# Performance work log

Hardware: AMD Instinct MI355X
Metric: run time of the kernel (lower is better)

The kernel has to match this reference:

```python
import jax, jax.numpy as jnp
import numpy as np

B, S, D = 32, 512, 1024
H, DH = 16, 64
EPS, TEMP = 1e-7, 0.1
P_LOGIT_INIT = float(np.log(0.2) - np.log(0.8))  # init_min == init_max == 0.2


def setup_inputs() -> dict:
    key = jax.random.key(0)
    ks = jax.random.split(key, 10)
    x = jax.random.normal(ks[0], (B, S, D), dtype=jnp.float32)
    lengths_x = jax.random.randint(ks[1], (B,), 0, S - 1)
    lengths_x = lengths_x.at[0].set(S - 1)  # ensure max(lengths)+1 == S, as torch code assumes
    Wq = jax.random.normal(ks[2], (D, H * DH), dtype=jnp.float32) * 0.02
    Wk = jax.random.normal(ks[3], (D, H * DH), dtype=jnp.float32) * 0.02
    Wv = jax.random.normal(ks[4], (D, H * DH), dtype=jnp.float32) * 0.02
    Wo = jax.random.normal(ks[5], (H * DH, D), dtype=jnp.float32) * 0.02
    p_logits = jnp.full((4,), P_LOGIT_INIT, dtype=jnp.float32)  # q, k, v, o
    noise_q = jax.random.uniform(ks[6], (B, S, D), dtype=jnp.float32)
    noise_k = jax.random.uniform(ks[7], (B, S, D), dtype=jnp.float32)
    noise_v = jax.random.uniform(ks[8], (B, S, D), dtype=jnp.float32)
    noise_o = jax.random.uniform(ks[9], (B, S, H * DH), dtype=jnp.float32)
    return {"x": x, "lengths_x": lengths_x, "Wq": Wq, "Wk": Wk, "Wv": Wv,
            "Wo": Wo, "p_logits": p_logits, "noise_q": noise_q,
            "noise_k": noise_k, "noise_v": noise_v, "noise_o": noise_o}


def _concrete_dropout(x, p_logit, u):
    p = jax.nn.sigmoid(p_logit)
    drop_prob = jax.nn.sigmoid(
        (jnp.log(p + EPS) - jnp.log(1.0 - p + EPS)
         + jnp.log(u + EPS) - jnp.log(1.0 - u + EPS)) / TEMP)
    return x * (1.0 - drop_prob) / (1.0 - p)


def reference(x, lengths_x, Wq, Wk, Wv, Wo, p_logits, noise_q, noise_k, noise_v, noise_o):
    b, s, _ = x.shape
    q = (_concrete_dropout(x, p_logits[0], noise_q) @ Wq).reshape(b, s, H, DH)
    k = (_concrete_dropout(x, p_logits[1], noise_k) @ Wk).reshape(b, s, H, DH)
    v = (_concrete_dropout(x, p_logits[2], noise_v) @ Wv).reshape(b, s, H, DH)
    e = jnp.einsum('bxhd,byhd->bhxy', q, k) / np.sqrt(DH).astype(np.float32)
    # mask[b, i, j] = 1 iff i <= lengths[b] and j <= lengths[b]
    valid = jnp.arange(s)[None, :] <= lengths_x[:, None]          # [B, S]
    mask = (valid[:, :, None] & valid[:, None, :])[:, None, :, :]  # [B, 1, S, S]
    e = jnp.where(mask, e, jnp.float32(-1e10))
    alpha = jax.nn.softmax(e, axis=-1)                             # [B, H, S, S]
    out = jnp.einsum('bhxy,byhd->bxhd', alpha, v).reshape(b, s, H * DH)
    out = _concrete_dropout(out, p_logits[3], noise_o) @ Wo
    return jax.nn.relu(out), alpha
```

## Files before the change

kernel.cpp:

```cpp
#include <hip/hip_runtime.h>

constexpr int B_ = 32, S_ = 512, D_ = 1024, H_ = 16, DH_ = 64, HD_ = 1024;
constexpr int M_ = B_ * S_;
constexpr float EPS_ = 1e-7f;
constexpr float INV_TEMP_ = 10.0f;

typedef __attribute__((ext_vector_type(8))) short bf16x8;
typedef __attribute__((ext_vector_type(4))) short bf16x4;
typedef __attribute__((ext_vector_type(4))) float f32x4;
typedef __attribute__((ext_vector_type(8))) unsigned short us8;

__device__ __forceinline__ float sigm(float x) { return 1.0f / (1.0f + __expf(-x)); }

__device__ __forceinline__ unsigned short f2bf(float f) {
    unsigned u = __float_as_uint(f);
    unsigned r = (u + 0x7FFFu + ((u >> 16) & 1u)) >> 16;
    return (unsigned short)r;
}

#define GLL16(gp, lp) __builtin_amdgcn_global_load_lds( \
    (const __attribute__((address_space(1))) unsigned int*)(gp), \
    (__attribute__((address_space(3))) unsigned int*)(lp), 16, 0, 0)

__device__ __forceinline__ bf16x8 ldsfrag64(const unsigned short* base, int row, int k) {
    int slot = ((k >> 3) ^ (row & 7)) << 3;
    return *(const bf16x8*)(base + row * 64 + slot);
}

__global__ __launch_bounds__(256)
void cd_cast3_kernel(const float* __restrict__ x,
                     const float* __restrict__ nq, const float* __restrict__ nk,
                     const float* __restrict__ nv, const float* __restrict__ pl,
                     unsigned short* __restrict__ aq, unsigned short* __restrict__ ak,
                     unsigned short* __restrict__ av)
{
    size_t i0 = ((size_t)blockIdx.x * 256 + threadIdx.x) * 8;

    float c0[3], inv1mp[3];
#pragma unroll
    for (int j = 0; j < 3; ++j) {
        float p = sigm(pl[j]);
        c0[j] = __logf(p + EPS_) - __logf(1.0f - p + EPS_);
        inv1mp[j] = 1.0f / (1.0f - p);
    }

    float4 x0 = *(const float4*)(x + i0);
    float4 x1 = *(const float4*)(x + i0 + 4);
    float xv[8] = {x0.x, x0.y, x0.z, x0.w, x1.x, x1.y, x1.z, x1.w};

    const float* ns[3] = {nq, nk, nv};
    unsigned short* os[3] = {aq, ak, av};
#pragma unroll
    for (int j = 0; j < 3; ++j) {
        float4 u0 = *(const float4*)(ns[j] + i0);
        float4 u1 = *(const float4*)(ns[j] + i0 + 4);
        float uv[8] = {u0.x, u0.y, u0.z, u0.w, u1.x, u1.y, u1.z, u1.w};
        ushort out[8];
#pragma unroll
        for (int t = 0; t < 8; ++t) {
            float lt = (c0[j] + __logf(uv[t] + EPS_) - __logf(1.0f - uv[t] + EPS_)) * INV_TEMP_;
            float dpr = sigm(lt);
            out[t] = f2bf(xv[t] * (1.0f - dpr) * inv1mp[j]);
        }
        *(us8*)(os[j] + i0) = *(us8*)out;
    }
}

__global__ __launch_bounds__(256)
void wcast_t4_kernel(const float* __restrict__ W0, const float* __restrict__ W1,
                     const float* __restrict__ W2, const float* __restrict__ W3,
                     unsigned short* __restrict__ T0, unsigned short* __restrict__ T1,
                     unsigned short* __restrict__ T2, unsigned short* __restrict__ T3)
{
    __shared__ unsigned short t[64][72];
    int z = blockIdx.z;
    const float* W = (z & 2) ? ((z & 1) ? W3 : W2) : ((z & 1) ? W1 : W0);
    unsigned short* WT = (z & 2) ? ((z & 1) ? T3 : T2) : ((z & 1) ? T1 : T0);
    int kb = blockIdx.y * 64;
    int nb = blockIdx.x * 64;
    int tid = threadIdx.x;
#pragma unroll
    for (int i = 0; i < 4; ++i) {
        int idx = tid + i * 256;
        int r = idx >> 4, c4 = idx & 15;
        float4 v = *(const float4*)(W + (size_t)(kb + r) * 1024 + nb + c4 * 4);
        t[c4 * 4 + 0][r] = f2bf(v.x);
        t[c4 * 4 + 1][r] = f2bf(v.y);
        t[c4 * 4 + 2][r] = f2bf(v.z);
        t[c4 * 4 + 3][r] = f2bf(v.w);
    }
    __syncthreads();
#pragma unroll
    for (int i = 0; i < 4; ++i) {
        int idx = tid + i * 256;
        int r = idx >> 4, c4 = idx & 15;
        ushort4 o;
        o.x = t[r][c4 * 4 + 0];
        o.y = t[r][c4 * 4 + 1];
        o.z = t[r][c4 * 4 + 2];
        o.w = t[r][c4 * 4 + 3];
        *(ushort4*)(WT + (size_t)(nb + r) * 1024 + kb + c4 * 4) = o;
    }
}

__global__ __launch_bounds__(256)
void vtrans_kernel(const unsigned short* __restrict__ vb, unsigned short* __restrict__ vT)
{
    __shared__ unsigned short t[64][136];
    int bh = blockIdx.y, b = bh >> 4, h = bh & 15;
    int y0 = blockIdx.x * 128;
    int tid = threadIdx.x;
#pragma unroll
    for (int i = 0; i < 4; ++i) {
        int idx = tid + i * 256;
        int r = idx >> 3, d0 = (idx & 7) * 8;
        us8 v = *(const us8*)(vb + ((size_t)(b * 512 + y0 + r)) * 1024 + h * 64 + d0);
#pragma unroll
        for (int e = 0; e < 8; ++e) t[d0 + e][r] = v[e];
    }
    __syncthreads();
#pragma unroll
    for (int i = 0; i < 4; ++i) {
        int idx = tid + i * 256;
        int dr = idx >> 4, y4 = (idx & 15) * 8;
        us8 o = *(const us8*)&t[dr][y4];
        *(us8*)(vT + ((size_t)bh * 64 + dr) * 512 + y0 + y4) = o;
    }
}

template<bool RELU, bool BF16OUT>
__global__ __launch_bounds__(256, 3)
void gemm_bf16_kernel(const unsigned short* __restrict__ A,
                      const unsigned short* __restrict__ BT,
                      void* __restrict__ Cv)
{
    const size_t zo = (size_t)blockIdx.y;
    A  += zo * (size_t)M_ * HD_;
    BT += zo * (size_t)(1024 * 1024);

    __shared__ unsigned short As[128 * 32];
    __shared__ unsigned short Bs[128 * 32];

    int flat = blockIdx.x;
    int swz = (flat & 7) * 128 + (flat >> 3);
    int ntile = swz & 7, mtile = swz >> 3;
    int m0 = mtile * 128, n0 = ntile * 128;

    int tid = threadIdx.x;
    int w = tid >> 6, lane = tid & 63;
    int wm = w >> 1, wn = w & 1;

    f32x4 acc[4][4];
#pragma unroll
    for (int m = 0; m < 4; ++m)
#pragma unroll
        for (int n = 0; n < 4; ++n) acc[m][n] = (f32x4){0.f, 0.f, 0.f, 0.f};

    const unsigned short* Ag = A + (size_t)(m0 + w * 32 + (lane >> 2)) * 1024 + (lane & 3) * 8;
    const unsigned short* Bg = BT + (size_t)(n0 + w * 32 + (lane >> 2)) * 1024 + (lane & 3) * 8;
    unsigned short* AsW = As + (w * 32) * 32;
    unsigned short* BsW = Bs + (w * 32) * 32;

    const int arow = wm * 64 + (lane & 15);
    const int brow = wn * 64 + (lane & 15);
    const int koff = (lane >> 4) * 8;

    for (int k0 = 0; k0 < 1024; k0 += 32) {
        __syncthreads();
        GLL16(Ag + k0,             AsW);
        GLL16(Ag + k0 + 16 * 1024, AsW + 16 * 32);
        GLL16(Bg + k0,             BsW);
        GLL16(Bg + k0 + 16 * 1024, BsW + 16 * 32);
        __syncthreads();

        bf16x8 afr[4], bfr[4];
#pragma unroll
        for (int m = 0; m < 4; ++m)
            afr[m] = *(const bf16x8*)&As[(arow + m * 16) * 32 + koff];
#pragma unroll
        for (int n = 0; n < 4; ++n)
            bfr[n] = *(const bf16x8*)&Bs[(brow + n * 16) * 32 + koff];
#pragma unroll
        for (int m = 0; m < 4; ++m)
#pragma unroll
            for (int n = 0; n < 4; ++n)
                acc[m][n] = __builtin_amdgcn_mfma_f32_16x16x32_bf16(afr[m], bfr[n], acc[m][n], 0, 0, 0);
    }

    int cr = (lane >> 4) * 4, cc = lane & 15;
#pragma unroll
    for (int m = 0; m < 4; ++m)
#pragma unroll
        for (int n = 0; n < 4; ++n)
#pragma unroll
            for (int j = 0; j < 4; ++j) {
                int row = m0 + wm * 64 + m * 16 + cr + j;
                int col = n0 + wn * 64 + n * 16 + cc;
                float v = acc[m][n][j];
                if (RELU) v = fmaxf(v, 0.f);
                if (BF16OUT) ((unsigned short*)Cv)[zo * (size_t)M_ * HD_ + (size_t)row * 1024 + col] = f2bf(v);
                else         ((float*)Cv)[(size_t)row * 1024 + col] = v;
            }
}

__global__ __launch_bounds__(512, 2)
void fused_attn2_kernel(const unsigned short* __restrict__ qb,
                        const unsigned short* __restrict__ kb,
                        const unsigned short* __restrict__ vT,
                        const float* __restrict__ no,
                        const float* __restrict__ pl,
                        const int* __restrict__ lengths,
                        float* __restrict__ alpha,
                        unsigned short* __restrict__ Ao)
{
    const int bh = blockIdx.x;
    const int b = bh >> 4, h = bh & 15;
    const int tid = threadIdx.x;
    const int w = tid >> 6, lane = tid & 63;
    const int g = lane >> 4, li = lane & 15;
    const int len = lengths[b];

    __shared__ unsigned short Kall[512 * 64];
    __shared__ unsigned short Vall[8 * 64 * 64];
    __shared__ unsigned short Olb[128 * 72];

    const int sr = lane >> 3;
    const int sc = ((lane & 7) ^ sr) * 8;

    {
        const size_t kbase = ((size_t)(b * 512 + w * 64)) * 1024 + h * 64;
        const size_t vbase = ((size_t)bh * 64) * 512;
#pragma unroll
        for (int c = 0; c < 8; ++c) {
            GLL16(kb + kbase + (size_t)(c * 8 + sr) * 1024 + sc, Kall + w * 4096 + c * 512);
            GLL16(vT + vbase + (size_t)(c * 8 + sr) * 512 + w * 64 + sc, Vall + w * 4096 + c * 512);
        }
    }
    __syncthreads();

    const float po = sigm(pl[3]);
    const float c0o = __logf(po + EPS_) - __logf(1.0f - po + EPS_);
    const float inv1mpo = 1.0f / (1.0f - po);

    for (int qt = 0; qt < 4; ++qt) {
        const int xg = qt * 128 + w * 16 + li;

        const unsigned short* qp = qb + ((size_t)(b * 512 + xg)) * 1024 + h * 64 + g * 8;
        bf16x8 qf0 = *(const bf16x8*)qp;
        bf16x8 qf1 = *(const bf16x8*)(qp + 32);

        f32x4 acc[32];
#pragma unroll
        for (int f = 0; f < 32; ++f) acc[f] = (f32x4){0.f, 0.f, 0.f, 0.f};

#pragma unroll
        for (int f = 0; f < 32; ++f) {
            bf16x8 kf0 = ldsfrag64(Kall, f * 16 + li, g * 8);
            bf16x8 kf1 = ldsfrag64(Kall, f * 16 + li, g * 8 + 32);
            acc[f] = __builtin_amdgcn_mfma_f32_16x16x32_bf16(kf0, qf0, acc[f], 0, 0, 0);
            acc[f] = __builtin_amdgcn_mfma_f32_16x16x32_bf16(kf1, qf1, acc[f], 0, 0, 0);
        }

        const bool vx = (xg <= len);
        float mx = -3.4e38f;
#pragma unroll
        for (int f = 0; f < 32; ++f)
#pragma unroll
            for (int r = 0; r < 4; ++r) {
                int y = f * 16 + g * 4 + r;
                float s = (vx && (y <= len)) ? acc[f][r] * 0.125f : -1e10f;
                acc[f][r] = s;
                mx = fmaxf(mx, s);
            }
        mx = fmaxf(mx, __shfl_xor(mx, 16));
        mx = fmaxf(mx, __shfl_xor(mx, 32));
        float sum = 0.f;
#pragma unroll
        for (int f = 0; f < 32; ++f)
#pragma unroll
            for (int r = 0; r < 4; ++r) {
                float e = __expf(acc[f][r] - mx);
                acc[f][r] = e;
                sum += e;
            }
        sum += __shfl_xor(sum, 16);
        sum += __shfl_xor(sum, 32);
        const float inv = 1.0f / sum;

        float* arow = alpha + ((size_t)bh * 512 + xg) * 512;
#pragma unroll
        for (int f = 0; f < 32; ++f) {
            f32x4 av = acc[f];
            av[0] *= inv; av[1] *= inv; av[2] *= inv; av[3] *= inv;
            acc[f] = av;
            *(float4*)(arow + f * 16 + g * 4) = make_float4(av[0], av[1], av[2], av[3]);
        }

        f32x4 acco[4];
#pragma unroll
        for (int cf = 0; cf < 4; ++cf) acco[cf] = (f32x4){0.f, 0.f, 0.f, 0.f};

#pragma unroll
        for (int yt = 0; yt < 8; ++yt) {
            const unsigned short* Vc = Vall + yt * 4096;
#pragma unroll
            for (int w2 = 0; w2 < 2; ++w2) {
                int f0 = yt * 4 + w2 * 2;
                bf16x8 pf;
#pragma unroll
                for (int r = 0; r < 4; ++r) {
                    pf[r]     = (short)f2bf(acc[f0][r]);
                    pf[4 + r] = (short)f2bf(acc[f0 + 1][r]);
                }
#pragma unroll
                for (int cf = 0; cf < 4; ++cf) {
                    int d = cf * 16 + li;
                    int s0 = w2 * 8 + g;
                    int s1 = s0 + 4;
                    int p0 = (((s0 >> 1) ^ (d & 7)) << 3) + ((s0 & 1) << 2);
                    int p1 = (((s1 >> 1) ^ (d & 7)) << 3) + ((s1 & 1) << 2);
                    bf16x4 lo = *(const bf16x4*)(Vc + d * 64 + p0);
                    bf16x4 hi = *(const bf16x4*)(Vc + d * 64 + p1);
                    bf16x8 vf;
#pragma unroll
                    for (int e = 0; e < 4; ++e) { vf[e] = lo[e]; vf[4 + e] = hi[e]; }
                    acco[cf] = __builtin_amdgcn_mfma_f32_16x16x32_bf16(pf, vf, acco[cf], 0, 0, 0);
                }
            }
        }

#pragma unroll
        for (int cf = 0; cf < 4; ++cf)
#pragma unroll
            for (int r = 0; r < 4; ++r)
                Olb[(w * 16 + g * 4 + r) * 72 + cf * 16 + li] = f2bf(acco[cf][r]);
        __syncthreads();

#pragma unroll
        for (int i = 0; i < 2; ++i) {
            int idx = tid + i * 512;
            int xr = idx >> 3, d0 = (idx & 7) * 8;
            int xglob = qt * 128 + xr;
            const float* nop = no + ((size_t)(b * 512 + xglob)) * 1024 + h * 64 + d0;
            float4 n0 = *(const float4*)nop;
            float4 n1 = *(const float4*)(nop + 4);
            float nn[8] = {n0.x, n0.y, n0.z, n0.w, n1.x, n1.y, n1.z, n1.w};
            us8 ov = *(const us8*)&Olb[xr * 72 + d0];
            ushort o[8];
#pragma unroll
            for (int e = 0; e < 8; ++e) {
                float val = __uint_as_float(((unsigned)ov[e]) << 16);
                float lt = (c0o + __logf(nn[e] + EPS_) - __logf(1.0f - nn[e] + EPS_)) * INV_TEMP_;
                o[e] = f2bf(val * (1.0f - sigm(lt)) * inv1mpo);
            }
            *(us8*)(Ao + ((size_t)(b * 512 + xglob)) * 1024 + h * 64 + d0) = *(us8*)o;
        }
        __syncthreads();
    }
}

extern "C" void kernel_launch(void* const* d_in, const int* in_sizes, int n_in,
                              void* d_out, int out_size, void* d_ws, size_t ws_size,
                              hipStream_t stream)
{
    const float* x       = (const float*)d_in[0];
    const int*   lengths = (const int*)d_in[1];
    const float* Wq      = (const float*)d_in[2];
    const float* Wk      = (const float*)d_in[3];
    const float* Wv      = (const float*)d_in[4];
    const float* Wo      = (const float*)d_in[5];
    const float* pl      = (const float*)d_in[6];
    const float* nq      = (const float*)d_in[7];
    const float* nk      = (const float*)d_in[8];
    const float* nv      = (const float*)d_in[9];
    const float* no      = (const float*)d_in[10];

    float* outp   = (float*)d_out;
    float* alphaF = outp + (size_t)M_ * D_;

    const size_t chunk = (size_t)M_ * HD_;
    unsigned short* qb  = (unsigned short*)d_ws;
    unsigned short* kb  = qb + chunk;
    unsigned short* vb  = kb + chunk;
    unsigned short* vT  = vb + chunk;
    unsigned short* Ao  = vT + chunk;
    unsigned short* WTo = Ao + chunk;

    unsigned short* WTq = (unsigned short*)(alphaF);
    unsigned short* Aq  = (unsigned short*)(alphaF + 1572864);
    unsigned short* WTk = WTq + (size_t)1024 * 1024;
    unsigned short* WTv = WTk + (size_t)1024 * 1024;

    dim3 blk(256);
    wcast_t4_kernel<<<dim3(16, 16, 4), blk, 0, stream>>>(Wq, Wk, Wv, Wo, WTq, WTk, WTv, WTo);

    cd_cast3_kernel<<<8192, blk, 0, stream>>>(x, nq, nk, nv, pl, Aq, Aq + chunk, Aq + 2 * chunk);

    gemm_bf16_kernel<false, true><<<dim3(1024, 3), blk, 0, stream>>>(Aq, WTq, qb);

    vtrans_kernel<<<dim3(4, 512), blk, 0, stream>>>(vb, vT);

    fused_attn2_kernel<<<512, 512, 0, stream>>>(qb, kb, vT, no, pl, lengths, alphaF, Ao);

    gemm_bf16_kernel<true, false><<<dim3(1024, 1), blk, 0, stream>>>(Ao, WTo, outp);
}
```

Before: 487.6 us.

## Fuse V transpose into QKV GEMM epilogue with LDS-staged vectorized stores

The QKV projection GEMM now stages its output tile through LDS and writes 16-byte vector stores. For the V slice it writes directly in transposed per-head layout, which removes the separate vtrans kernel and its global round trip. The alpha stores in attention become nontemporal, and the output GEMM is specialized with ReLU. The epilogue gains extra LDS traffic and barriers, and the shared LDS buffer grows.

```diff
diff --git a/kernel.cpp b/kernel.cpp
--- a/kernel.cpp
+++ b/kernel.cpp
@@ -103,43 +103,19 @@
     }
 }
 
-__global__ __launch_bounds__(256)
-void vtrans_kernel(const unsigned short* __restrict__ vb, unsigned short* __restrict__ vT)
-{
-    __shared__ unsigned short t[64][136];
-    int bh = blockIdx.y, b = bh >> 4, h = bh & 15;
-    int y0 = blockIdx.x * 128;
-    int tid = threadIdx.x;
-#pragma unroll
-    for (int i = 0; i < 4; ++i) {
-        int idx = tid + i * 256;
-        int r = idx >> 3, d0 = (idx & 7) * 8;
-        us8 v = *(const us8*)(vb + ((size_t)(b * 512 + y0 + r)) * 1024 + h * 64 + d0);
-#pragma unroll
-        for (int e = 0; e < 8; ++e) t[d0 + e][r] = v[e];
-    }
-    __syncthreads();
-#pragma unroll
-    for (int i = 0; i < 4; ++i) {
-        int idx = tid + i * 256;
-        int dr = idx >> 4, y4 = (idx & 15) * 8;
-        us8 o = *(const us8*)&t[dr][y4];
-        *(us8*)(vT + ((size_t)bh * 64 + dr) * 512 + y0 + y4) = o;
-    }
-}
-
-template<bool RELU, bool BF16OUT>
 __global__ __launch_bounds__(256, 3)
-void gemm_bf16_kernel(const unsigned short* __restrict__ A,
-                      const unsigned short* __restrict__ BT,
-                      void* __restrict__ Cv)
-{
-    const size_t zo = (size_t)blockIdx.y;
-    A  += zo * (size_t)M_ * HD_;
-    BT += zo * (size_t)(1024 * 1024);
-
-    __shared__ unsigned short As[128 * 32];
-    __shared__ unsigned short Bs[128 * 32];
+void gemm_qkv_kernel(const unsigned short* __restrict__ A,
+                     const unsigned short* __restrict__ BT,
+                     unsigned short* __restrict__ qkb,
+                     unsigned short* __restrict__ vT)
+{
+    const int zo = blockIdx.y;
+    A  += (size_t)zo * M_ * HD_;
+    BT += (size_t)zo * (1024 * 1024);
+
+    __shared__ unsigned short LDSU[8704];
+    unsigned short* As = LDSU;
+    unsigned short* Bs = LDSU + 4096;
 
     int flat = blockIdx.x;
     int swz = (flat & 7) * 128 + (flat >> 3);
@@ -187,6 +163,104 @@
                 acc[m][n] = __builtin_amdgcn_mfma_f32_16x16x32_bf16(afr[m], bfr[n], acc[m][n], 0, 0, 0);
     }
 
+    const int cr = (lane >> 4) * 4, cc = lane & 15;
+    __syncthreads();
+
+    if (zo < 2) {
+        unsigned short* Cb = qkb + (size_t)zo * M_ * HD_;
+        for (int n = 0; n < 4; ++n) {
+#pragma unroll
+            for (int m = 0; m < 4; ++m)
+#pragma unroll
+                for (int j = 0; j < 4; ++j)
+                    LDSU[(wm * 64 + m * 16 + cr + j) * 68 + wn * 16 + cc] = f2bf(acc[m][n][j]);
+            __syncthreads();
+#pragma unroll
+            for (int t = 0; t < 2; ++t) {
+                int fl = tid + t * 256;
+                int row = fl >> 2, p = fl & 3;
+                us8 vv = *(const us8*)&LDSU[row * 68 + p * 8];
+                int colg = n0 + (p >> 1) * 64 + n * 16 + (p & 1) * 8;
+                *(us8*)(Cb + (size_t)(m0 + row) * 1024 + colg) = vv;
+            }
+            __syncthreads();
+        }
+    } else {
+        int b = m0 >> 9, y0 = m0 & 511, h0 = n0 >> 6;
+        for (int n = 0; n < 4; ++n) {
+#pragma unroll
+            for (int m = 0; m < 4; ++m)
+#pragma unroll
+                for (int j = 0; j < 4; ++j)
+                    LDSU[(wn * 16 + cc) * 132 + wm * 64 + m * 16 + cr + j] = f2bf(acc[m][n][j]);
+            __syncthreads();
+#pragma unroll
+            for (int t = 0; t < 2; ++t) {
+                int fl = tid + t * 256;
+                int cl = fl >> 4, yp = fl & 15;
+                us8 vv = *(const us8*)&LDSU[cl * 132 + yp * 8];
+                int h = h0 + (cl >> 4), d = n * 16 + (cl & 15);
+                *(us8*)(vT + ((size_t)((b * 16 + h) * 64 + d)) * 512 + y0 + yp * 8) = vv;
+            }
+            __syncthreads();
+        }
+    }
+}
+
+__global__ __launch_bounds__(256, 3)
+void gemm_o_kernel(const unsigned short* __restrict__ A,
+                   const unsigned short* __restrict__ BT,
+                   float* __restrict__ C)
+{
+    __shared__ unsigned short As[128 * 32];
+    __shared__ unsigned short Bs[128 * 32];
+
+    int flat = blockIdx.x;
+    int swz = (flat & 7) * 128 + (flat >> 3);
+    int ntile = swz & 7, mtile = swz >> 3;
+    int m0 = mtile * 128, n0 = ntile * 128;
+
+    int tid = threadIdx.x;
+    int w = tid >> 6, lane = tid & 63;
+    int wm = w >> 1, wn = w & 1;
+
+    f32x4 acc[4][4];
+#pragma unroll
+    for (int m = 0; m < 4; ++m)
+#pragma unroll
+        for (int n = 0; n < 4; ++n) acc[m][n] = (f32x4){0.f, 0.f, 0.f, 0.f};
+
+    const unsigned short* Ag = A + (size_t)(m0 + w * 32 + (lane >> 2)) * 1024 + (lane & 3) * 8;
+    const unsigned short* Bg = BT + (size_t)(n0 + w * 32 + (lane >> 2)) * 1024 + (lane & 3) * 8;
+    unsigned short* AsW = As + (w * 32) * 32;
+    unsigned short* BsW = Bs + (w * 32) * 32;
+
+    const int arow = wm * 64 + (lane & 15);
+    const int brow = wn * 64 + (lane & 15);
+    const int koff = (lane >> 4) * 8;
+
+    for (int k0 = 0; k0 < 1024; k0 += 32) {
+        __syncthreads();
+        GLL16(Ag + k0,             AsW);
+        GLL16(Ag + k0 + 16 * 1024, AsW + 16 * 32);
+        GLL16(Bg + k0,             BsW);
+        GLL16(Bg + k0 + 16 * 1024, BsW + 16 * 32);
+        __syncthreads();
+
+        bf16x8 afr[4], bfr[4];
+#pragma unroll
+        for (int m = 0; m < 4; ++m)
+            afr[m] = *(const bf16x8*)&As[(arow + m * 16) * 32 + koff];
+#pragma unroll
+        for (int n = 0; n < 4; ++n)
+            bfr[n] = *(const bf16x8*)&Bs[(brow + n * 16) * 32 + koff];
+#pragma unroll
+        for (int m = 0; m < 4; ++m)
+#pragma unroll
+            for (int n = 0; n < 4; ++n)
+                acc[m][n] = __builtin_amdgcn_mfma_f32_16x16x32_bf16(afr[m], bfr[n], acc[m][n], 0, 0, 0);
+    }
+
     int cr = (lane >> 4) * 4, cc = lane & 15;
 #pragma unroll
     for (int m = 0; m < 4; ++m)
@@ -196,10 +270,7 @@
             for (int j = 0; j < 4; ++j) {
                 int row = m0 + wm * 64 + m * 16 + cr + j;
                 int col = n0 + wn * 64 + n * 16 + cc;
-                float v = acc[m][n][j];
-                if (RELU) v = fmaxf(v, 0.f);
-                if (BF16OUT) ((unsigned short*)Cv)[zo * (size_t)M_ * HD_ + (size_t)row * 1024 + col] = f2bf(v);
-                else         ((float*)Cv)[(size_t)row * 1024 + col] = v;
+                C[(size_t)row * 1024 + col] = fmaxf(acc[m][n][j], 0.f);
             }
 }
 
@@ -293,7 +364,7 @@
             f32x4 av = acc[f];
             av[0] *= inv; av[1] *= inv; av[2] *= inv; av[3] *= inv;
             acc[f] = av;
-            *(float4*)(arow + f * 16 + g * 4) = make_float4(av[0], av[1], av[2], av[3]);
+            __builtin_nontemporal_store(av, (f32x4*)(arow + f * 16 + g * 4));
         }
 
         f32x4 acco[4];
@@ -381,8 +452,7 @@
     const size_t chunk = (size_t)M_ * HD_;
     unsigned short* qb  = (unsigned short*)d_ws;
     unsigned short* kb  = qb + chunk;
-    unsigned short* vb  = kb + chunk;
-    unsigned short* vT  = vb + chunk;
+    unsigned short* vT  = kb + chunk;
     unsigned short* Ao  = vT + chunk;
     unsigned short* WTo = Ao + chunk;
 
@@ -396,11 +466,9 @@
 
     cd_cast3_kernel<<<8192, blk, 0, stream>>>(x, nq, nk, nv, pl, Aq, Aq + chunk, Aq + 2 * chunk);
 
-    gemm_bf16_kernel<false, true><<<dim3(1024, 3), blk, 0, stream>>>(Aq, WTq, qb);
-
-    vtrans_kernel<<<dim3(4, 512), blk, 0, stream>>>(vb, vT);
+    gemm_qkv_kernel<<<dim3(1024, 3), blk, 0, stream>>>(Aq, WTq, qb, vT);
 
     fused_attn2_kernel<<<512, 512, 0, stream>>>(qb, kb, vT, no, pl, lengths, alphaF, Ao);
 
-    gemm_bf16_kernel<true, false><<<dim3(1024, 1), blk, 0, stream>>>(Ao, WTo, outp);
-}
+    gemm_o_kernel<<<1024, blk, 0, stream>>>(Ao, WTo, outp);
+}
```

Measured after the change: 482.1 us, median of 2. Within noise of the previous version (-1.1%).
